# Kernel optimization log

Hardware: AMD Instinct MI355X
Metric: run time of the kernel (lower is better)

## Reference

```python
import jax, jax.numpy as jnp
import numpy as np

GROUP_SIZE = 128
TOP_K = 2
ZERO_POINT = 8  # Marlin symmetric zero point: w = scale * (q - 8)


def _dequant_int4(q, scales, group_size):
    # q: [E, N, K] int values in [0,15]; scales: [E, N, K//group_size]
    s = jnp.repeat(scales, group_size, axis=-1)  # [E, N, K]
    return (q.astype(jnp.float32) - float(ZERO_POINT)) * s


def setup_inputs() -> dict:
    key = jax.random.key(0)
    k1, k2, k3, k4, k5, k6 = jax.random.split(key, 6)
    B, S, H, I, E = 2, 1024, 2048, 1408, 8
    router_logits = jax.random.normal(k1, (B, S, E), dtype=jnp.float32)
    hidden_states = jax.random.normal(k2, (B, S, H), dtype=jnp.float32)
    fc_gate_up_qweights = jax.random.randint(k3, (E, 2 * I, H), 0, 16, dtype=jnp.int32)
    fc_gate_up_scales = jax.random.uniform(k4, (E, 2 * I, H // GROUP_SIZE), dtype=jnp.float32) * 0.02
    fc_down_qweights = jax.random.randint(k5, (E, H, I), 0, 16, dtype=jnp.int32)
    fc_down_scales = jax.random.uniform(k6, (E, H, I // GROUP_SIZE), dtype=jnp.float32) * 0.02
    return {
        "router_logits": router_logits,
        "hidden_states": hidden_states,
        "fc_gate_up_qweights": fc_gate_up_qweights,
        "fc_gate_up_scales": fc_gate_up_scales,
        "fc_down_qweights": fc_down_qweights,
        "fc_down_scales": fc_down_scales,
    }


def reference(router_logits, hidden_states, fc_gate_up_qweights, fc_gate_up_scales,
              fc_down_qweights, fc_down_scales):
    B, S, H = hidden_states.shape
    E = router_logits.shape[-1]
    T = B * S
    x = hidden_states.reshape(T, H)
    logits = router_logits.reshape(T, E)

    # top-k routing with softmax over selected logits
    top_vals, top_idx = jax.lax.top_k(logits, TOP_K)          # [T, k]
    top_w = jax.nn.softmax(top_vals, axis=-1)                 # [T, k]
    route_w = jnp.zeros((T, E), x.dtype).at[jnp.arange(T)[:, None], top_idx].set(top_w)  # [T, E]

    # dequantize int4 weights: scale * (q - 8), per-group along K
    w_gate_up = _dequant_int4(fc_gate_up_qweights, fc_gate_up_scales, GROUP_SIZE)  # [E, 2I, H]
    w_down = _dequant_int4(fc_down_qweights, fc_down_scales, GROUP_SIZE)          # [E, H, I]

    # grouped GEMM (dense over experts, masked by routing weights)
    gu = jnp.einsum('th,enh->ten', x, w_gate_up)              # [T, E, 2I]
    gate, up = jnp.split(gu, 2, axis=-1)
    act = jax.nn.silu(gate) * up                              # SwiGLU, [T, E, I]
    out = jnp.einsum('tei,ehi,te->th', act, w_down, route_w)  # [T, H]
    return out.reshape(B, S, H)
```

## Files before the change

kernel.cpp:

```cpp
#include <hip/hip_runtime.h>
#include <hip/hip_bf16.h>

#define T_TOKENS 2048
#define H_DIM    2048
#define I_DIM    1408
#define E_NUM    8

typedef __bf16 bf16;
typedef __attribute__((ext_vector_type(8))) __bf16  bf16x8;
typedef __attribute__((ext_vector_type(4))) float   floatx4;

static const size_t OFF_COUNTS = 0;
static const size_t OFF_LISTS  = 256;
static const size_t OFF_WLISTS = OFF_LISTS + (size_t)T_TOKENS * E_NUM * 4;
static const size_t OFF_XB     = 131328;
static const size_t OFF_ACT    = OFF_XB + (size_t)T_TOKENS * H_DIM * 2;
static const size_t OFF_GUPK   = OFF_ACT + (size_t)2 * T_TOKENS * I_DIM * 2;
static const size_t OFF_DNPK   = OFF_GUPK + (size_t)E_NUM * 22 * 32 * 16384;
static const size_t OFF_TMP    = OFF_GUPK;

__global__ __launch_bounds__(256) void pack_gu_kernel(const int* __restrict__ q,
                                                      const float* __restrict__ sc,
                                                      bf16* __restrict__ out)
{
    const int b = blockIdx.x;
    const int t = threadIdx.x;
    const int e = b / 2816;
    const int grow = b - e * 2816;
    const int4* qp = reinterpret_cast<const int4*>(q + (size_t)b * H_DIM) + t * 2;
    int4 a = qp[0], c = qp[1];
    float s = sc[(size_t)b * 16 + (t >> 4)];
    float m8s = -8.f * s;
    bf16x8 bv;
    bv[0] = (bf16)fmaf((float)a.x, s, m8s);
    bv[1] = (bf16)fmaf((float)a.y, s, m8s);
    bv[2] = (bf16)fmaf((float)a.z, s, m8s);
    bv[3] = (bf16)fmaf((float)a.w, s, m8s);
    bv[4] = (bf16)fmaf((float)c.x, s, m8s);
    bv[5] = (bf16)fmaf((float)c.y, s, m8s);
    bv[6] = (bf16)fmaf((float)c.z, s, m8s);
    bv[7] = (bf16)fmaf((float)c.w, s, m8s);
    const int is_up = grow >= I_DIM;
    const int icol  = grow - (is_up ? I_DIM : 0);
    const int nt    = icol >> 6;
    const int r     = ((((icol >> 4) & 3) * 2 + is_up) * 16) + (icol & 15);
    size_t dst = ((((size_t)e * 22 + nt) * 32 + (t >> 3)) * 128 + r) * 8 + ((t & 7) ^ (r & 7));
    reinterpret_cast<bf16x8*>(out)[dst] = bv;
}

__global__ __launch_bounds__(256) void pack_dn_kernel(const int* __restrict__ q,
                                                      const float* __restrict__ sc,
                                                      bf16* __restrict__ out)
{
    const int b = blockIdx.x;
    const int t = threadIdx.x;
    if (t >= 176) return;
    const int e = b >> 11;
    const int grow = b & 2047;
    const int4* qp = reinterpret_cast<const int4*>(q + (size_t)b * I_DIM) + t * 2;
    int4 a = qp[0], c = qp[1];
    float s = sc[(size_t)b * 11 + (t >> 4)];
    float m8s = -8.f * s;
    bf16x8 bv;
    bv[0] = (bf16)fmaf((float)a.x, s, m8s);
    bv[1] = (bf16)fmaf((float)a.y, s, m8s);
    bv[2] = (bf16)fmaf((float)a.z, s, m8s);
    bv[3] = (bf16)fmaf((float)a.w, s, m8s);
    bv[4] = (bf16)fmaf((float)c.x, s, m8s);
    bv[5] = (bf16)fmaf((float)c.y, s, m8s);
    bv[6] = (bf16)fmaf((float)c.z, s, m8s);
    bv[7] = (bf16)fmaf((float)c.w, s, m8s);
    const int nt = grow >> 7;
    const int r  = grow & 127;
    size_t dst = ((((size_t)e * 16 + nt) * 22 + (t >> 3)) * 128 + r) * 8 + ((t & 7) ^ (r & 7));
    reinterpret_cast<bf16x8*>(out)[dst] = bv;
}

__global__ void xconv_kernel(const float* __restrict__ x, bf16* __restrict__ xb)
{
    int i = blockIdx.x * blockDim.x + threadIdx.x;
    const float4* x4 = reinterpret_cast<const float4*>(x) + (size_t)i * 2;
    float4 v0 = x4[0], v1 = x4[1];
    bf16x8 bv;
    bv[0] = (bf16)v0.x; bv[1] = (bf16)v0.y; bv[2] = (bf16)v0.z; bv[3] = (bf16)v0.w;
    bv[4] = (bf16)v1.x; bv[5] = (bf16)v1.y; bv[6] = (bf16)v1.z; bv[7] = (bf16)v1.w;
    *reinterpret_cast<bf16x8*>(xb + (size_t)i * 8) = bv;
}

__global__ void router_kernel(const float* __restrict__ logits,
                              int* __restrict__ counts,
                              int* __restrict__ lists,
                              float* __restrict__ wlists)
{
    int t = blockIdx.x * blockDim.x + threadIdx.x;
    if (t >= T_TOKENS) return;
    const float* l = logits + (size_t)t * E_NUM;
    float v0 = -1e30f, v1 = -1e30f;
    int i0 = 0, i1 = 0;
    #pragma unroll
    for (int e = 0; e < E_NUM; ++e) {
        float v = l[e];
        if (v > v0) { v1 = v0; i1 = i0; v0 = v; i0 = e; }
        else if (v > v1) { v1 = v; i1 = e; }
    }
    float w0 = 1.f / (1.f + __expf(v1 - v0));
    float w1 = 1.f - w0;
    int p0 = atomicAdd(&counts[i0], 1);
    lists[i0 * T_TOKENS + p0] = t * 2 + 0;
    wlists[i0 * T_TOKENS + p0] = w0;
    int p1 = atomicAdd(&counts[i1], 1);
    lists[i1 * T_TOKENS + p1] = t * 2 + 1;
    wlists[i1 * T_TOKENS + p1] = w1;
}

__global__ __launch_bounds__(256) void gemm1_kernel(
    const bf16* __restrict__ xb,
    const bf16* __restrict__ wpk,
    const int*  __restrict__ counts,
    const int*  __restrict__ lists,
    bf16*       __restrict__ act)
{
    const int e   = blockIdx.z;
    const int cnt = counts[e];
    const int m0  = blockIdx.y * 128;
    if (m0 >= cnt) return;
    const int nt  = blockIdx.x;

    __shared__ __align__(16) bf16 Al[8192];
    __shared__ __align__(16) bf16 Bl[8192];
    __shared__ int meta[128];

    const int tid = threadIdx.x;
    if (tid < 128) {
        int m = m0 + tid;
        meta[tid] = lists[e * T_TOKENS + (m < cnt ? m : 0)];
    }
    __syncthreads();

    const int lane = tid & 63;
    const int wv = tid >> 6;
    const int wm = wv >> 1, wn = wv & 1;

    int    aoff[4];
    size_t agbl[4];
    #pragma unroll
    for (int j = 0; j < 4; ++j) {
        int g = tid + 256 * j;
        int arow = g >> 3, cg = g & 7;
        aoff[j] = arow * 64 + ((cg ^ (arow & 7)) * 8);
        agbl[j] = (size_t)(meta[arow] >> 1) * H_DIM + cg * 8;
    }
    const bf16* bt = wpk + ((size_t)e * 22 + nt) * (32 * 8192) + tid * 8;

    int afr[2][4], bfr[2][4];
    #pragma unroll
    for (int ks = 0; ks < 2; ++ks) {
        int gidx = ks * 4 + (lane >> 4);
        #pragma unroll
        for (int t4 = 0; t4 < 4; ++t4) {
            int ra = wm * 64 + t4 * 16 + (lane & 15);
            afr[ks][t4] = ra * 64 + ((gidx ^ (ra & 7)) * 8);
            int rb = wn * 64 + t4 * 16 + (lane & 15);
            bfr[ks][t4] = rb * 64 + ((gidx ^ (rb & 7)) * 8);
        }
    }

    floatx4 acc[4][4];
    #pragma unroll
    for (int i = 0; i < 4; ++i)
        #pragma unroll
        for (int j = 0; j < 4; ++j)
            acc[i][j] = (floatx4){0.f, 0.f, 0.f, 0.f};

    for (int k0 = 0; k0 < H_DIM; k0 += 64) {
        #pragma unroll
        for (int j = 0; j < 4; ++j) {
            bf16x8 v = *reinterpret_cast<const bf16x8*>(xb + agbl[j] + k0);
            *reinterpret_cast<bf16x8*>(&Al[aoff[j]]) = v;
        }
        const bf16* bsrc = bt + (size_t)(k0 >> 6) * 8192;
        #pragma unroll
        for (int j = 0; j < 4; ++j) {
            bf16x8 v = *reinterpret_cast<const bf16x8*>(bsrc + j * 2048);
            *reinterpret_cast<bf16x8*>(&Bl[tid * 8 + j * 2048]) = v;
        }
        __syncthreads();
        #pragma unroll
        for (int ks = 0; ks < 2; ++ks) {
            bf16x8 af[4], bff[4];
            #pragma unroll
            for (int mt = 0; mt < 4; ++mt)
                af[mt] = *reinterpret_cast<const bf16x8*>(&Al[afr[ks][mt]]);
            #pragma unroll
            for (int ntf = 0; ntf < 4; ++ntf)
                bff[ntf] = *reinterpret_cast<const bf16x8*>(&Bl[bfr[ks][ntf]]);
            #pragma unroll
            for (int mt = 0; mt < 4; ++mt)
                #pragma unroll
                for (int ntf = 0; ntf < 4; ++ntf)
                    acc[mt][ntf] = __builtin_amdgcn_mfma_f32_16x16x32_bf16(af[mt], bff[ntf], acc[mt][ntf], 0, 0, 0);
        }
        __syncthreads();
    }

    const int rbase = (lane >> 4) * 4;
    const int cn = lane & 15;
    #pragma unroll
    for (int mt = 0; mt < 4; ++mt) {
        #pragma unroll
        for (int j = 0; j < 2; ++j) {
            floatx4 g = acc[mt][2 * j];
            floatx4 u = acc[mt][2 * j + 1];
            int col = nt * 64 + (wn * 2 + j) * 16 + cn;
            #pragma unroll
            for (int r = 0; r < 4; ++r) {
                int lrow = wm * 64 + mt * 16 + rbase + r;
                if (m0 + lrow < cnt) {
                    float gate = g[r], up = u[r];
                    float a = gate / (1.f + __expf(-gate)) * up;
                    act[(size_t)meta[lrow] * I_DIM + col] = (bf16)a;
                }
            }
        }
    }
}

__global__ __launch_bounds__(256) void gemm2_kernel(
    const bf16*  __restrict__ act,
    const bf16*  __restrict__ wpk,
    const int*   __restrict__ counts,
    const int*   __restrict__ lists,
    const float* __restrict__ wlists,
    float*       __restrict__ tmp)
{
    const int e   = blockIdx.z;
    const int cnt = counts[e];
    const int m0  = blockIdx.y * 128;
    if (m0 >= cnt) return;
    const int nt  = blockIdx.x;

    __shared__ __align__(16) bf16 Al[8192];
    __shared__ __align__(16) bf16 Bl[8192];
    __shared__ int   meta[128];
    __shared__ float wmeta[128];

    const int tid = threadIdx.x;
    if (tid < 128) {
        int m = m0 + tid;
        int mm = (m < cnt) ? m : 0;
        meta[tid]  = lists[e * T_TOKENS + mm];
        wmeta[tid] = wlists[e * T_TOKENS + mm];
    }
    __syncthreads();

    const int lane = tid & 63;
    const int wv = tid >> 6;
    const int wm = wv >> 1, wn = wv & 1;

    int    aoff[4];
    size_t agbl[4];
    #pragma unroll
    for (int j = 0; j < 4; ++j) {
        int g = tid + 256 * j;
        int arow = g >> 3, cg = g & 7;
        aoff[j] = arow * 64 + ((cg ^ (arow & 7)) * 8);
        agbl[j] = (size_t)meta[arow] * I_DIM + cg * 8;
    }
    const bf16* bt = wpk + ((size_t)e * 16 + nt) * (22 * 8192) + tid * 8;

    int afr[2][4], bfr[2][4];
    #pragma unroll
    for (int ks = 0; ks < 2; ++ks) {
        int gidx = ks * 4 + (lane >> 4);
        #pragma unroll
        for (int t4 = 0; t4 < 4; ++t4) {
            int ra = wm * 64 + t4 * 16 + (lane & 15);
            afr[ks][t4] = ra * 64 + ((gidx ^ (ra & 7)) * 8);
            int rb = wn * 64 + t4 * 16 + (lane & 15);
            bfr[ks][t4] = rb * 64 + ((gidx ^ (rb & 7)) * 8);
        }
    }

    floatx4 acc[4][4];
    #pragma unroll
    for (int i = 0; i < 4; ++i)
        #pragma unroll
        for (int j = 0; j < 4; ++j)
            acc[i][j] = (floatx4){0.f, 0.f, 0.f, 0.f};

    for (int kt = 0; kt < 22; ++kt) {
        #pragma unroll
        for (int j = 0; j < 4; ++j) {
            bf16x8 v = *reinterpret_cast<const bf16x8*>(act + agbl[j] + kt * 64);
            *reinterpret_cast<bf16x8*>(&Al[aoff[j]]) = v;
        }
        const bf16* bsrc = bt + (size_t)kt * 8192;
        #pragma unroll
        for (int j = 0; j < 4; ++j) {
            bf16x8 v = *reinterpret_cast<const bf16x8*>(bsrc + j * 2048);
            *reinterpret_cast<bf16x8*>(&Bl[tid * 8 + j * 2048]) = v;
        }
        __syncthreads();
        #pragma unroll
        for (int ks = 0; ks < 2; ++ks) {
            bf16x8 af[4], bff[4];
            #pragma unroll
            for (int mt = 0; mt < 4; ++mt)
                af[mt] = *reinterpret_cast<const bf16x8*>(&Al[afr[ks][mt]]);
            #pragma unroll
            for (int ntf = 0; ntf < 4; ++ntf)
                bff[ntf] = *reinterpret_cast<const bf16x8*>(&Bl[bfr[ks][ntf]]);
            #pragma unroll
            for (int mt = 0; mt < 4; ++mt)
                #pragma unroll
                for (int ntf = 0; ntf < 4; ++ntf)
                    acc[mt][ntf] = __builtin_amdgcn_mfma_f32_16x16x32_bf16(af[mt], bff[ntf], acc[mt][ntf], 0, 0, 0);
        }
        __syncthreads();
    }

    const int rbase = (lane >> 4) * 4;
    const int cn = lane & 15;
    #pragma unroll
    for (int mt = 0; mt < 4; ++mt) {
        #pragma unroll
        for (int ntf = 0; ntf < 4; ++ntf) {
            floatx4 v = acc[mt][ntf];
            int col = nt * 128 + wn * 64 + ntf * 16 + cn;
            #pragma unroll
            for (int r = 0; r < 4; ++r) {
                int lrow = wm * 64 + mt * 16 + rbase + r;
                if (m0 + lrow < cnt) {
                    tmp[(size_t)meta[lrow] * H_DIM + col] = wmeta[lrow] * v[r];
                }
            }
        }
    }
}

__global__ void finalize_kernel(const float* __restrict__ tmp, float* __restrict__ out)
{
    int i4 = blockIdx.x * blockDim.x + threadIdx.x;
    int t  = i4 >> 9;
    int h  = (i4 & 511) * 4;
    float4 a = *reinterpret_cast<const float4*>(tmp + ((size_t)2 * t) * H_DIM + h);
    float4 b = *reinterpret_cast<const float4*>(tmp + ((size_t)(2 * t + 1)) * H_DIM + h);
    float4 o;
    o.x = a.x + b.x; o.y = a.y + b.y; o.z = a.z + b.z; o.w = a.w + b.w;
    *reinterpret_cast<float4*>(out + (size_t)t * H_DIM + h) = o;
}

extern "C" void kernel_launch(void* const* d_in, const int* in_sizes, int n_in,
                              void* d_out, int out_size, void* d_ws, size_t ws_size,
                              hipStream_t stream)
{
    const float* router_logits = (const float*)d_in[0];
    const float* x             = (const float*)d_in[1];
    const int*   gu_q          = (const int*)d_in[2];
    const float* gu_s          = (const float*)d_in[3];
    const int*   dn_q          = (const int*)d_in[4];
    const float* dn_s          = (const float*)d_in[5];
    float* out = (float*)d_out;

    char* ws = (char*)d_ws;
    int*   counts = (int*)(ws + OFF_COUNTS);
    int*   lists  = (int*)(ws + OFF_LISTS);
    float* wlists = (float*)(ws + OFF_WLISTS);
    bf16*  xb     = (bf16*)(ws + OFF_XB);
    bf16*  act    = (bf16*)(ws + OFF_ACT);
    bf16*  gu_pk  = (bf16*)(ws + OFF_GUPK);
    bf16*  dn_pk  = (bf16*)(ws + OFF_DNPK);
    float* tmp    = (float*)(ws + OFF_TMP);

    hipMemsetAsync(counts, 0, E_NUM * sizeof(int), stream);

    pack_gu_kernel<<<E_NUM * 2816, 256, 0, stream>>>(gu_q, gu_s, gu_pk);
    pack_dn_kernel<<<E_NUM * 2048, 256, 0, stream>>>(dn_q, dn_s, dn_pk);
    xconv_kernel<<<T_TOKENS * H_DIM / 8 / 256, 256, 0, stream>>>(x, xb);
    router_kernel<<<T_TOKENS / 256, 256, 0, stream>>>(router_logits, counts, lists, wlists);

    gemm1_kernel<<<dim3(22, 16, 8), 256, 0, stream>>>(xb, gu_pk, counts, lists, act);
    gemm2_kernel<<<dim3(16, 16, 8), 256, 0, stream>>>(act, dn_pk, counts, lists, wlists, tmp);
    finalize_kernel<<<4096, 256, 0, stream>>>(tmp, out);
}
```

Before: 523.4 us.

## Fuse int4 dequant into grouped GEMMs with async LDS loads and 256-row tiles

Removes the separate weight pack kernels and dequantizes the int32-stored int4 weights directly inside both grouped GEMMs. The next tile's weights are prefetched into registers while the current tile is converted and written to LDS. Activation rows now go straight to LDS through global_load_lds, the M tile grows from 128 to 256 rows, and block indices are remapped so experts interleave across the grid. This drops the round trip through the bf16 packed-weight buffers. In exchange, each M tile re-reads and re-dequantizes the weights, and the larger accumulator raises register pressure.

```diff
diff --git a/kernel.cpp b/kernel.cpp
--- a/kernel.cpp
+++ b/kernel.cpp
@@ -9,72 +9,28 @@
 typedef __bf16 bf16;
 typedef __attribute__((ext_vector_type(8))) __bf16  bf16x8;
 typedef __attribute__((ext_vector_type(4))) float   floatx4;
+
+#define MFMA __builtin_amdgcn_mfma_f32_16x16x32_bf16
 
 static const size_t OFF_COUNTS = 0;
 static const size_t OFF_LISTS  = 256;
 static const size_t OFF_WLISTS = OFF_LISTS + (size_t)T_TOKENS * E_NUM * 4;
 static const size_t OFF_XB     = 131328;
 static const size_t OFF_ACT    = OFF_XB + (size_t)T_TOKENS * H_DIM * 2;
-static const size_t OFF_GUPK   = OFF_ACT + (size_t)2 * T_TOKENS * I_DIM * 2;
-static const size_t OFF_DNPK   = OFF_GUPK + (size_t)E_NUM * 22 * 32 * 16384;
-static const size_t OFF_TMP    = OFF_GUPK;
-
-__global__ __launch_bounds__(256) void pack_gu_kernel(const int* __restrict__ q,
-                                                      const float* __restrict__ sc,
-                                                      bf16* __restrict__ out)
-{
-    const int b = blockIdx.x;
-    const int t = threadIdx.x;
-    const int e = b / 2816;
-    const int grow = b - e * 2816;
-    const int4* qp = reinterpret_cast<const int4*>(q + (size_t)b * H_DIM) + t * 2;
-    int4 a = qp[0], c = qp[1];
-    float s = sc[(size_t)b * 16 + (t >> 4)];
-    float m8s = -8.f * s;
-    bf16x8 bv;
-    bv[0] = (bf16)fmaf((float)a.x, s, m8s);
-    bv[1] = (bf16)fmaf((float)a.y, s, m8s);
-    bv[2] = (bf16)fmaf((float)a.z, s, m8s);
-    bv[3] = (bf16)fmaf((float)a.w, s, m8s);
-    bv[4] = (bf16)fmaf((float)c.x, s, m8s);
-    bv[5] = (bf16)fmaf((float)c.y, s, m8s);
-    bv[6] = (bf16)fmaf((float)c.z, s, m8s);
-    bv[7] = (bf16)fmaf((float)c.w, s, m8s);
-    const int is_up = grow >= I_DIM;
-    const int icol  = grow - (is_up ? I_DIM : 0);
-    const int nt    = icol >> 6;
-    const int r     = ((((icol >> 4) & 3) * 2 + is_up) * 16) + (icol & 15);
-    size_t dst = ((((size_t)e * 22 + nt) * 32 + (t >> 3)) * 128 + r) * 8 + ((t & 7) ^ (r & 7));
-    reinterpret_cast<bf16x8*>(out)[dst] = bv;
-}
-
-__global__ __launch_bounds__(256) void pack_dn_kernel(const int* __restrict__ q,
-                                                      const float* __restrict__ sc,
-                                                      bf16* __restrict__ out)
-{
-    const int b = blockIdx.x;
-    const int t = threadIdx.x;
-    if (t >= 176) return;
-    const int e = b >> 11;
-    const int grow = b & 2047;
-    const int4* qp = reinterpret_cast<const int4*>(q + (size_t)b * I_DIM) + t * 2;
-    int4 a = qp[0], c = qp[1];
-    float s = sc[(size_t)b * 11 + (t >> 4)];
-    float m8s = -8.f * s;
-    bf16x8 bv;
-    bv[0] = (bf16)fmaf((float)a.x, s, m8s);
-    bv[1] = (bf16)fmaf((float)a.y, s, m8s);
-    bv[2] = (bf16)fmaf((float)a.z, s, m8s);
-    bv[3] = (bf16)fmaf((float)a.w, s, m8s);
-    bv[4] = (bf16)fmaf((float)c.x, s, m8s);
-    bv[5] = (bf16)fmaf((float)c.y, s, m8s);
-    bv[6] = (bf16)fmaf((float)c.z, s, m8s);
-    bv[7] = (bf16)fmaf((float)c.w, s, m8s);
-    const int nt = grow >> 7;
-    const int r  = grow & 127;
-    size_t dst = ((((size_t)e * 16 + nt) * 22 + (t >> 3)) * 128 + r) * 8 + ((t & 7) ^ (r & 7));
-    reinterpret_cast<bf16x8*>(out)[dst] = bv;
-}
+static const size_t OFF_TMP    = OFF_ACT + (size_t)2 * T_TOKENS * I_DIM * 2;
+
+__device__ __forceinline__ void gload_lds16(const bf16* g, bf16* l)
+{
+    __builtin_amdgcn_global_load_lds((const __attribute__((address_space(1))) void*)g,
+                                     (__attribute__((address_space(3))) void*)l,
+                                     16, 0, 0);
+}
+
+#define PHASE_BAR() do { __builtin_amdgcn_sched_barrier(0); \
+                         __builtin_amdgcn_s_barrier(); \
+                         __builtin_amdgcn_sched_barrier(0); } while (0)
+
+#define RD(buf, row, g8) (*reinterpret_cast<const bf16x8*>(&(buf)[(row) * 64 + (g8)]))
 
 __global__ void xconv_kernel(const float* __restrict__ x, bf16* __restrict__ xb)
 {
@@ -113,25 +69,28 @@
     wlists[i1 * T_TOKENS + p1] = w1;
 }
 
-__global__ __launch_bounds__(256) void gemm1_kernel(
-    const bf16* __restrict__ xb,
-    const bf16* __restrict__ wpk,
-    const int*  __restrict__ counts,
-    const int*  __restrict__ lists,
-    bf16*       __restrict__ act)
-{
-    const int e   = blockIdx.z;
+__global__ __launch_bounds__(256, 2) void gemm1_kernel(
+    const bf16*  __restrict__ xb,
+    const int*   __restrict__ q,
+    const float* __restrict__ sc,
+    const int*   __restrict__ counts,
+    const int*   __restrict__ lists,
+    bf16*        __restrict__ act)
+{
+    const int lid = (blockIdx.x & 7) * 176 + (blockIdx.x >> 3);
+    const int e   = lid / 176;
+    const int r_  = lid - e * 176;
+    const int nt  = r_ >> 3;
+    const int m0  = (r_ & 7) << 8;
     const int cnt = counts[e];
-    const int m0  = blockIdx.y * 128;
     if (m0 >= cnt) return;
-    const int nt  = blockIdx.x;
-
-    __shared__ __align__(16) bf16 Al[8192];
+
+    __shared__ __align__(16) bf16 Al[16384];
     __shared__ __align__(16) bf16 Bl[8192];
-    __shared__ int meta[128];
+    __shared__ int meta[256];
 
     const int tid = threadIdx.x;
-    if (tid < 128) {
+    if (tid < 256) {
         int m = m0 + tid;
         meta[tid] = lists[e * T_TOKENS + (m < cnt ? m : 0)];
     }
@@ -141,111 +100,154 @@
     const int wv = tid >> 6;
     const int wm = wv >> 1, wn = wv & 1;
 
-    int    aoff[4];
-    size_t agbl[4];
+    const int gB = (tid & 7) ^ ((tid >> 3) & 7);
+
+    size_t aglb[8];
+    #pragma unroll
+    for (int j = 0; j < 8; ++j)
+        aglb[j] = (size_t)(meta[(tid >> 3) + 32 * j] >> 1) * H_DIM + gB * 8;
+
+    const int*   qb_[4];
+    const float* sb_[4];
     #pragma unroll
     for (int j = 0; j < 4; ++j) {
-        int g = tid + 256 * j;
-        int arow = g >> 3, cg = g & 7;
-        aoff[j] = arow * 64 + ((cg ^ (arow & 7)) * 8);
-        agbl[j] = (size_t)(meta[arow] >> 1) * H_DIM + cg * 8;
-    }
-    const bf16* bt = wpk + ((size_t)e * 22 + nt) * (32 * 8192) + tid * 8;
-
-    int afr[2][4], bfr[2][4];
-    #pragma unroll
-    for (int ks = 0; ks < 2; ++ks) {
-        int gidx = ks * 4 + (lane >> 4);
-        #pragma unroll
-        for (int t4 = 0; t4 < 4; ++t4) {
-            int ra = wm * 64 + t4 * 16 + (lane & 15);
-            afr[ks][t4] = ra * 64 + ((gidx ^ (ra & 7)) * 8);
-            int rb = wn * 64 + t4 * 16 + (lane & 15);
-            bfr[ks][t4] = rb * 64 + ((gidx ^ (rb & 7)) * 8);
-        }
-    }
-
-    floatx4 acc[4][4];
-    #pragma unroll
-    for (int i = 0; i < 4; ++i)
+        int r     = (tid >> 3) + 32 * j;
+        int t16   = r >> 4;
+        int is_up = t16 & 1;
+        int icol  = nt * 64 + (t16 >> 1) * 16 + (r & 15);
+        int row_q = e * 2816 + (is_up ? I_DIM : 0) + icol;
+        qb_[j] = q  + (size_t)row_q * H_DIM + gB * 8;
+        sb_[j] = sc + (size_t)row_q * 16;
+    }
+
+    floatx4 acc[8][4];
+    #pragma unroll
+    for (int i = 0; i < 8; ++i)
         #pragma unroll
         for (int j = 0; j < 4; ++j)
             acc[i][j] = (floatx4){0.f, 0.f, 0.f, 0.f};
 
-    for (int k0 = 0; k0 < H_DIM; k0 += 64) {
+    int4  qv[8];
+    float scv[4];
+    #pragma unroll
+    for (int j = 0; j < 4; ++j) {
+        const int4* p = reinterpret_cast<const int4*>(qb_[j]);
+        qv[2 * j]     = p[0];
+        qv[2 * j + 1] = p[1];
+        scv[j]        = sb_[j][0];
+    }
+
+    const int l15   = lane & 15;
+    const int g80   = (((lane >> 4) ^ (lane & 7)) << 3);
+    const int g81   = g80 ^ 32;
+    const int abase = wm * 128 + l15;
+    const int bbase = wn * 64 + l15;
+
+    for (int kt = 0; kt < 32; ++kt) {
+        const int k0 = kt * 64;
+        #pragma unroll
+        for (int j = 0; j < 8; ++j)
+            gload_lds16(xb + aglb[j] + k0, &Al[(tid + 256 * j) * 8]);
+
+        asm volatile("s_waitcnt vmcnt(8)" ::: "memory");
+
         #pragma unroll
         for (int j = 0; j < 4; ++j) {
-            bf16x8 v = *reinterpret_cast<const bf16x8*>(xb + agbl[j] + k0);
-            *reinterpret_cast<bf16x8*>(&Al[aoff[j]]) = v;
-        }
-        const bf16* bsrc = bt + (size_t)(k0 >> 6) * 8192;
-        #pragma unroll
-        for (int j = 0; j < 4; ++j) {
-            bf16x8 v = *reinterpret_cast<const bf16x8*>(bsrc + j * 2048);
-            *reinterpret_cast<bf16x8*>(&Bl[tid * 8 + j * 2048]) = v;
-        }
-        __syncthreads();
+            float s = scv[j], m8 = -8.f * s;
+            int4 a = qv[2 * j], b = qv[2 * j + 1];
+            bf16x8 bv;
+            bv[0] = (bf16)fmaf((float)a.x, s, m8);
+            bv[1] = (bf16)fmaf((float)a.y, s, m8);
+            bv[2] = (bf16)fmaf((float)a.z, s, m8);
+            bv[3] = (bf16)fmaf((float)a.w, s, m8);
+            bv[4] = (bf16)fmaf((float)b.x, s, m8);
+            bv[5] = (bf16)fmaf((float)b.y, s, m8);
+            bv[6] = (bf16)fmaf((float)b.z, s, m8);
+            bv[7] = (bf16)fmaf((float)b.w, s, m8);
+            *reinterpret_cast<bf16x8*>(&Bl[(tid + 256 * j) * 8]) = bv;
+        }
+
+        if (kt < 31) {
+            const int koff = k0 + 64;
+            const int grp  = (kt + 1) >> 1;
+            #pragma unroll
+            for (int j = 0; j < 4; ++j) {
+                const int4* p = reinterpret_cast<const int4*>(qb_[j] + koff);
+                qv[2 * j]     = p[0];
+                qv[2 * j + 1] = p[1];
+                scv[j]        = sb_[j][grp];
+            }
+            asm volatile("s_waitcnt vmcnt(12)" ::: "memory");
+        } else {
+            asm volatile("s_waitcnt vmcnt(0)" ::: "memory");
+        }
+        asm volatile("s_waitcnt lgkmcnt(0)" ::: "memory");
+        PHASE_BAR();
+
         #pragma unroll
         for (int ks = 0; ks < 2; ++ks) {
-            bf16x8 af[4], bff[4];
-            #pragma unroll
-            for (int mt = 0; mt < 4; ++mt)
-                af[mt] = *reinterpret_cast<const bf16x8*>(&Al[afr[ks][mt]]);
-            #pragma unroll
-            for (int ntf = 0; ntf < 4; ++ntf)
-                bff[ntf] = *reinterpret_cast<const bf16x8*>(&Bl[bfr[ks][ntf]]);
-            #pragma unroll
-            for (int mt = 0; mt < 4; ++mt)
+            const int g8 = ks ? g81 : g80;
+            bf16x8 bf_[4];
+            #pragma unroll
+            for (int nf = 0; nf < 4; ++nf)
+                bf_[nf] = RD(Bl, bbase + nf * 16, g8);
+            #pragma unroll
+            for (int mt = 0; mt < 8; ++mt) {
+                bf16x8 af = RD(Al, abase + mt * 16, g8);
                 #pragma unroll
-                for (int ntf = 0; ntf < 4; ++ntf)
-                    acc[mt][ntf] = __builtin_amdgcn_mfma_f32_16x16x32_bf16(af[mt], bff[ntf], acc[mt][ntf], 0, 0, 0);
-        }
-        __syncthreads();
+                for (int nf = 0; nf < 4; ++nf)
+                    acc[mt][nf] = MFMA(af, bf_[nf], acc[mt][nf], 0, 0, 0);
+            }
+        }
+        PHASE_BAR();
     }
 
     const int rbase = (lane >> 4) * 4;
     const int cn = lane & 15;
     #pragma unroll
-    for (int mt = 0; mt < 4; ++mt) {
-        #pragma unroll
-        for (int j = 0; j < 2; ++j) {
-            floatx4 g = acc[mt][2 * j];
-            floatx4 u = acc[mt][2 * j + 1];
-            int col = nt * 64 + (wn * 2 + j) * 16 + cn;
+    for (int mt = 0; mt < 8; ++mt) {
+        #pragma unroll
+        for (int qd = 0; qd < 2; ++qd) {
+            floatx4 g = acc[mt][2 * qd];
+            floatx4 u = acc[mt][2 * qd + 1];
+            int col = nt * 64 + (wn * 2 + qd) * 16 + cn;
             #pragma unroll
             for (int r = 0; r < 4; ++r) {
-                int lrow = wm * 64 + mt * 16 + rbase + r;
+                int lrow = wm * 128 + mt * 16 + rbase + r;
                 if (m0 + lrow < cnt) {
                     float gate = g[r], up = u[r];
-                    float a = gate / (1.f + __expf(-gate)) * up;
-                    act[(size_t)meta[lrow] * I_DIM + col] = (bf16)a;
+                    float av = gate / (1.f + __expf(-gate)) * up;
+                    act[(size_t)meta[lrow] * I_DIM + col] = (bf16)av;
                 }
             }
         }
     }
 }
 
-__global__ __launch_bounds__(256) void gemm2_kernel(
+__global__ __launch_bounds__(256, 2) void gemm2_kernel(
     const bf16*  __restrict__ act,
-    const bf16*  __restrict__ wpk,
+    const int*   __restrict__ q,
+    const float* __restrict__ sc,
     const int*   __restrict__ counts,
     const int*   __restrict__ lists,
     const float* __restrict__ wlists,
     float*       __restrict__ tmp)
 {
-    const int e   = blockIdx.z;
+    const int lid = (blockIdx.x & 7) * 128 + (blockIdx.x >> 3);
+    const int e   = lid >> 7;
+    const int r_  = lid & 127;
+    const int nt  = r_ >> 3;
+    const int m0  = (r_ & 7) << 8;
     const int cnt = counts[e];
-    const int m0  = blockIdx.y * 128;
     if (m0 >= cnt) return;
-    const int nt  = blockIdx.x;
-
-    __shared__ __align__(16) bf16 Al[8192];
+
+    __shared__ __align__(16) bf16 Al[16384];
     __shared__ __align__(16) bf16 Bl[8192];
-    __shared__ int   meta[128];
-    __shared__ float wmeta[128];
+    __shared__ int   meta[256];
+    __shared__ float wmeta[256];
 
     const int tid = threadIdx.x;
-    if (tid < 128) {
+    if (tid < 256) {
         int m = m0 + tid;
         int mm = (m < cnt) ? m : 0;
         meta[tid]  = lists[e * T_TOKENS + mm];
@@ -257,79 +259,116 @@
     const int wv = tid >> 6;
     const int wm = wv >> 1, wn = wv & 1;
 
-    int    aoff[4];
-    size_t agbl[4];
+    const int gB = (tid & 7) ^ ((tid >> 3) & 7);
+
+    size_t aglb[8];
+    #pragma unroll
+    for (int j = 0; j < 8; ++j)
+        aglb[j] = (size_t)meta[(tid >> 3) + 32 * j] * I_DIM + gB * 8;
+
+    const int*   qb_[4];
+    const float* sb_[4];
     #pragma unroll
     for (int j = 0; j < 4; ++j) {
-        int g = tid + 256 * j;
-        int arow = g >> 3, cg = g & 7;
-        aoff[j] = arow * 64 + ((cg ^ (arow & 7)) * 8);
-        agbl[j] = (size_t)meta[arow] * I_DIM + cg * 8;
-    }
-    const bf16* bt = wpk + ((size_t)e * 16 + nt) * (22 * 8192) + tid * 8;
-
-    int afr[2][4], bfr[2][4];
-    #pragma unroll
-    for (int ks = 0; ks < 2; ++ks) {
-        int gidx = ks * 4 + (lane >> 4);
-        #pragma unroll
-        for (int t4 = 0; t4 < 4; ++t4) {
-            int ra = wm * 64 + t4 * 16 + (lane & 15);
-            afr[ks][t4] = ra * 64 + ((gidx ^ (ra & 7)) * 8);
-            int rb = wn * 64 + t4 * 16 + (lane & 15);
-            bfr[ks][t4] = rb * 64 + ((gidx ^ (rb & 7)) * 8);
-        }
-    }
-
-    floatx4 acc[4][4];
-    #pragma unroll
-    for (int i = 0; i < 4; ++i)
+        int r     = (tid >> 3) + 32 * j;
+        int row_q = e * 2048 + nt * 128 + r;
+        qb_[j] = q  + (size_t)row_q * I_DIM + gB * 8;
+        sb_[j] = sc + (size_t)row_q * 11;
+    }
+
+    floatx4 acc[8][4];
+    #pragma unroll
+    for (int i = 0; i < 8; ++i)
         #pragma unroll
         for (int j = 0; j < 4; ++j)
             acc[i][j] = (floatx4){0.f, 0.f, 0.f, 0.f};
 
+    int4  qv[8];
+    float scv[4];
+    #pragma unroll
+    for (int j = 0; j < 4; ++j) {
+        const int4* p = reinterpret_cast<const int4*>(qb_[j]);
+        qv[2 * j]     = p[0];
+        qv[2 * j + 1] = p[1];
+        scv[j]        = sb_[j][0];
+    }
+
+    const int l15   = lane & 15;
+    const int g80   = (((lane >> 4) ^ (lane & 7)) << 3);
+    const int g81   = g80 ^ 32;
+    const int abase = wm * 128 + l15;
+    const int bbase = wn * 64 + l15;
+
     for (int kt = 0; kt < 22; ++kt) {
+        const int k0 = kt * 64;
+        #pragma unroll
+        for (int j = 0; j < 8; ++j)
+            gload_lds16(act + aglb[j] + k0, &Al[(tid + 256 * j) * 8]);
+
+        asm volatile("s_waitcnt vmcnt(8)" ::: "memory");
+
         #pragma unroll
         for (int j = 0; j < 4; ++j) {
-            bf16x8 v = *reinterpret_cast<const bf16x8*>(act + agbl[j] + kt * 64);
-            *reinterpret_cast<bf16x8*>(&Al[aoff[j]]) = v;
-        }
-        const bf16* bsrc = bt + (size_t)kt * 8192;
-        #pragma unroll
-        for (int j = 0; j < 4; ++j) {
-            bf16x8 v = *reinterpret_cast<const bf16x8*>(bsrc + j * 2048);
-            *reinterpret_cast<bf16x8*>(&Bl[tid * 8 + j * 2048]) = v;
-        }
-        __syncthreads();
+            float s = scv[j], m8 = -8.f * s;
+            int4 a = qv[2 * j], b = qv[2 * j + 1];
+            bf16x8 bv;
+            bv[0] = (bf16)fmaf((float)a.x, s, m8);
+            bv[1] = (bf16)fmaf((float)a.y, s, m8);
+            bv[2] = (bf16)fmaf((float)a.z, s, m8);
+            bv[3] = (bf16)fmaf((float)a.w, s, m8);
+            bv[4] = (bf16)fmaf((float)b.x, s, m8);
+            bv[5] = (bf16)fmaf((float)b.y, s, m8);
+            bv[6] = (bf16)fmaf((float)b.z, s, m8);
+            bv[7] = (bf16)fmaf((float)b.w, s, m8);
+            *reinterpret_cast<bf16x8*>(&Bl[(tid + 256 * j) * 8]) = bv;
+        }
+
+        if (kt < 21) {
+            const int koff = k0 + 64;
+            const int grp  = (kt + 1) >> 1;
+            #pragma unroll
+            for (int j = 0; j < 4; ++j) {
+                const int4* p = reinterpret_cast<const int4*>(qb_[j] + koff);
+                qv[2 * j]     = p[0];
+                qv[2 * j + 1] = p[1];
+                scv[j]        = sb_[j][grp];
+            }
+            asm volatile("s_waitcnt vmcnt(12)" ::: "memory");
+        } else {
+            asm volatile("s_waitcnt vmcnt(0)" ::: "memory");
+        }
+        asm volatile("s_waitcnt lgkmcnt(0)" ::: "memory");
+        PHASE_BAR();
+
         #pragma unroll
         for (int ks = 0; ks < 2; ++ks) {
-            bf16x8 af[4], bff[4];
-            #pragma unroll
-            for (int mt = 0; mt < 4; ++mt)
-                af[mt] = *reinterpret_cast<const bf16x8*>(&Al[afr[ks][mt]]);
-            #pragma unroll
-            for (int ntf = 0; ntf < 4; ++ntf)
-                bff[ntf] = *reinterpret_cast<const bf16x8*>(&Bl[bfr[ks][ntf]]);
-            #pragma unroll
-            for (int mt = 0; mt < 4; ++mt)
+            const int g8 = ks ? g81 : g80;
+            bf16x8 bf_[4];
+            #pragma unroll
+            for (int nf = 0; nf < 4; ++nf)
+                bf_[nf] = RD(Bl, bbase + nf * 16, g8);
+            #pragma unroll
+            for (int mt = 0; mt < 8; ++mt) {
+                bf16x8 af = RD(Al, abase + mt * 16, g8);
                 #pragma unroll
-                for (int ntf = 0; ntf < 4; ++ntf)
-                    acc[mt][ntf] = __builtin_amdgcn_mfma_f32_16x16x32_bf16(af[mt], bff[ntf], acc[mt][ntf], 0, 0, 0);
-        }
-        __syncthreads();
+                for (int nf = 0; nf < 4; ++nf)
+                    acc[mt][nf] = MFMA(af, bf_[nf], acc[mt][nf], 0, 0, 0);
+            }
+        }
+        PHASE_BAR();
     }
 
     const int rbase = (lane >> 4) * 4;
     const int cn = lane & 15;
     #pragma unroll
-    for (int mt = 0; mt < 4; ++mt) {
-        #pragma unroll
-        for (int ntf = 0; ntf < 4; ++ntf) {
-            floatx4 v = acc[mt][ntf];
-            int col = nt * 128 + wn * 64 + ntf * 16 + cn;
+    for (int mt = 0; mt < 8; ++mt) {
+        #pragma unroll
+        for (int nf = 0; nf < 4; ++nf) {
+            floatx4 v = acc[mt][nf];
+            int col = nt * 128 + wn * 64 + nf * 16 + cn;
             #pragma unroll
             for (int r = 0; r < 4; ++r) {
-                int lrow = wm * 64 + mt * 16 + rbase + r;
+                int lrow = wm * 128 + mt * 16 + rbase + r;
                 if (m0 + lrow < cnt) {
                     tmp[(size_t)meta[lrow] * H_DIM + col] = wmeta[lrow] * v[r];
                 }
@@ -368,18 +407,14 @@
     float* wlists = (float*)(ws + OFF_WLISTS);
     bf16*  xb     = (bf16*)(ws + OFF_XB);
     bf16*  act    = (bf16*)(ws + OFF_ACT);
-    bf16*  gu_pk  = (bf16*)(ws + OFF_GUPK);
-    bf16*  dn_pk  = (bf16*)(ws + OFF_DNPK);
     float* tmp    = (float*)(ws + OFF_TMP);
 
     hipMemsetAsync(counts, 0, E_NUM * sizeof(int), stream);
 
-    pack_gu_kernel<<<E_NUM * 2816, 256, 0, stream>>>(gu_q, gu_s, gu_pk);
-    pack_dn_kernel<<<E_NUM * 2048, 256, 0, stream>>>(dn_q, dn_s, dn_pk);
     xconv_kernel<<<T_TOKENS * H_DIM / 8 / 256, 256, 0, stream>>>(x, xb);
     router_kernel<<<T_TOKENS / 256, 256, 0, stream>>>(router_logits, counts, lists, wlists);
 
-    gemm1_kernel<<<dim3(22, 16, 8), 256, 0, stream>>>(xb, gu_pk, counts, lists, act);
-    gemm2_kernel<<<dim3(16, 16, 8), 256, 0, stream>>>(act, dn_pk, counts, lists, wlists, tmp);
+    gemm1_kernel<<<176 * E_NUM, 256, 0, stream>>>(xb, gu_q, gu_s, counts, lists, act);
+    gemm2_kernel<<<128 * E_NUM, 256, 0, stream>>>(act, dn_q, dn_s, counts, lists, wlists, tmp);
     finalize_kernel<<<4096, 256, 0, stream>>>(tmp, out);
 }
```

Measured after the change: 577.1 us. +10.2%, slower.
